# Kernel tuning notes

Hardware: AMD Instinct MI355X
Metric: run time of the kernel (lower is better)

The kernel has to match this reference:

```python
import jax, jax.numpy as jnp
import numpy as np

N_NODES = 50000
N_EDGES = 800000
F_IN = 256
F_OUT = 256


def setup_inputs() -> dict:
    key = jax.random.key(0)
    k1, k2, k3, k4, k5 = jax.random.split(key, 5)
    x = jax.random.normal(k1, (N_NODES, F_IN), dtype=jnp.float32)
    edge_index = jax.random.randint(k2, (2, N_EDGES), 0, N_NODES, dtype=jnp.int64)
    C_values = jax.random.uniform(k3, (N_EDGES,), dtype=jnp.float32)
    # nn.Linear(input_dim, output_dim) parameters
    W = jax.random.normal(k4, (F_OUT, F_IN), dtype=jnp.float32) / np.sqrt(F_IN)
    b = jax.random.normal(k5, (F_OUT,), dtype=jnp.float32) * 0.01
    return {"x": x, "edge_index": edge_index, "C_values": C_values, "W": W, "b": b}


def reference(x, edge_index, C_values, W, b):
    # gcn_norm(add_self_loops=False): deg = row-sum of edge weights,
    # w_norm[e] = deg[row]^-1/2 * w[e] * deg[col]^-1/2
    row, col = edge_index[0], edge_index[1]
    n = x.shape[0]
    deg = jax.ops.segment_sum(C_values, row, num_segments=n)  # [N]
    deg_inv_sqrt = jnp.where(deg > 0, jax.lax.rsqrt(jnp.where(deg > 0, deg, 1.0)), 0.0)
    w_norm = deg_inv_sqrt[row] * C_values * deg_inv_sqrt[col]  # [E]
    # SpMM: prop_x[i] = sum_{e: row[e]=i} w_norm[e] * x[col[e]]
    prop_x = jax.ops.segment_sum(w_norm[:, None] * x[col], row, num_segments=n)  # [N, F_in]
    # dense linear transform
    return prop_x @ W.T + b  # [N, F_out]
```

## Files before the change

### kernel.cpp

```cpp
#include <hip/hip_runtime.h>
#include <hip/hip_bf16.h>

#define NN 50000
#define NE 800000
#define FD 256
#define NN_PAD 50048
#define SCAN_B 196
#define NPB 16

typedef __attribute__((ext_vector_type(8))) short bf16x8;
typedef __attribute__((ext_vector_type(4))) float f32x4;
typedef unsigned long long ull;

__device__ __forceinline__ short f2bf(float f) {
    union { float f; unsigned u; } v; v.f = f;
    unsigned r = v.u + 0x7fffu + ((v.u >> 16) & 1u);
    return (short)(r >> 16);
}
__device__ __forceinline__ float bf2f(unsigned short u) {
    union { unsigned u; float f; } v; v.u = ((unsigned)u) << 16;
    return v.f;
}

__global__ void count_deg_kernel(const int* __restrict__ row, const float* __restrict__ cv,
                                 ull* __restrict__ dc) {
    int e = blockIdx.x * blockDim.x + threadIdx.x;
    if (e < NE) {
        int r = row[e];
        unsigned cf = (unsigned)(cv[e] * 16777216.0f + 0.5f);
        atomicAdd(&dc[r], (1ULL << 40) | (ull)cf);
    }
}

__device__ __forceinline__ int block_excl_scan256(int v, int tid) {
    __shared__ int ws[4];
    int lane = tid & 63, wv = tid >> 6;
    int incl = v;
#pragma unroll
    for (int off = 1; off < 64; off <<= 1) {
        int t = __shfl_up(incl, off);
        if (lane >= off) incl += t;
    }
    if (lane == 63) ws[wv] = incl;
    __syncthreads();
    int acc = 0;
#pragma unroll
    for (int k = 0; k < 4; ++k) if (k < wv) acc += ws[k];
    return acc + incl - v;
}

__global__ void sum_dinv_kernel(const ull* __restrict__ dc, float* __restrict__ dinv,
                                int* __restrict__ bsum) {
    int i = blockIdx.x * 256 + threadIdx.x;
    ull v = (i < NN) ? dc[i] : 0ULL;
    int cnt = (int)(v >> 40);
    ull df = v & ((1ULL << 40) - 1);
    int lane = threadIdx.x & 63, wv = threadIdx.x >> 6;
    int s = cnt;
#pragma unroll
    for (int off = 1; off < 64; off <<= 1) s += __shfl_xor(s, off);
    __shared__ int ws[4];
    if (lane == 0) ws[wv] = s;
    __syncthreads();
    if (threadIdx.x == 0) bsum[blockIdx.x] = ws[0] + ws[1] + ws[2] + ws[3];
    if (i < NN) {
        float d = (float)df * (1.0f / 16777216.0f);
        dinv[i] = (df > 0) ? rsqrtf(d) : 0.f;
    }
}

__global__ void scan_bsum_kernel(int* __restrict__ bsum) {
    int tid = threadIdx.x;
    int v = (tid < SCAN_B) ? bsum[tid] : 0;
    int excl = block_excl_scan256(v, tid);
    if (tid < SCAN_B) bsum[tid] = excl;
}

__global__ void write_rs_kernel(const ull* __restrict__ dc, const int* __restrict__ bsum,
                                int* __restrict__ rs, int* __restrict__ cursor) {
    int i = blockIdx.x * 256 + threadIdx.x;
    int v = (i < NN) ? (int)(dc[i] >> 40) : 0;
    int excl = block_excl_scan256(v, threadIdx.x) + bsum[blockIdx.x];
    if (i < NN) { rs[i] = excl; cursor[i] = excl; }
    if (i == NN - 1) rs[NN] = excl + v;
}

__global__ void quant_kernel(const float* __restrict__ x, const float* __restrict__ W,
                             const float* __restrict__ dinv, unsigned* __restrict__ q8,
                             float* __restrict__ scale, short* __restrict__ Wb) {
    int wid = blockIdx.x * 4 + (threadIdx.x >> 6);
    int lane = threadIdx.x & 63;
    if (wid < NN) {
        int r = wid;
        float dr = dinv[r];
        float4 v = *(const float4*)(x + (size_t)r * FD + lane * 4);
        v.x *= dr; v.y *= dr; v.z *= dr; v.w *= dr;
        float m = fmaxf(fmaxf(fabsf(v.x), fabsf(v.y)), fmaxf(fabsf(v.z), fabsf(v.w)));
#pragma unroll
        for (int off = 1; off < 64; off <<= 1) m = fmaxf(m, __shfl_xor(m, off, 64));
        float s   = (m > 0.f) ? m * (1.0f / 127.0f) : 1.0f;
        float inv = (m > 0.f) ? 127.0f / m : 0.f;
        if (lane == 0) scale[r] = s;
        int q0 = (int)rintf(v.x * inv) + 128;
        int q1 = (int)rintf(v.y * inv) + 128;
        int q2 = (int)rintf(v.z * inv) + 128;
        int q3 = (int)rintf(v.w * inv) + 128;
        q8[r * 64 + lane] = (unsigned)q0 | ((unsigned)q1 << 8) |
                            ((unsigned)q2 << 16) | ((unsigned)q3 << 24);
    } else {
        int j = (wid - NN) * 64 + lane;
        if (j < FD * FD) Wb[j] = f2bf(W[j]);
    }
}

__global__ void bucket_kernel(const int* __restrict__ row, const int* __restrict__ col,
                              const float* __restrict__ cv, const float* __restrict__ scale,
                              int* __restrict__ cursor, unsigned* __restrict__ e_cw) {
    int e = blockIdx.x * blockDim.x + threadIdx.x;
    if (e >= NE) return;
    int r = row[e], c = col[e];
    float w = cv[e] * scale[c];
    int idx = atomicAdd(&cursor[r], 1);
    unsigned wb = (unsigned)(unsigned short)f2bf(w);
    e_cw[idx] = (wb << 16) | (unsigned)c;
}

__global__ __launch_bounds__(256) void fused_kernel(
        const unsigned* __restrict__ q8, const unsigned* __restrict__ e_cw,
        const int* __restrict__ rs, const float* __restrict__ dinv,
        const short* __restrict__ Wb, const float* __restrict__ bias,
        float* __restrict__ out) {
    __shared__ short Ab[NPB][264];
    int tid = threadIdx.x, lane = tid & 63, wv = tid >> 6;
    int q = lane >> 4, i = lane & 15;
    int nbase = blockIdx.x * NPB;
    int n = nbase + wv * 4 + q;

    int e = rs[n], en = rs[n + 1];
    const unsigned* xq = q8 + i * 4;

    float acc[16];
#pragma unroll
    for (int k = 0; k < 16; ++k) acc[k] = 0.f;
    float wsum = 0.f;

#define EDGE(V, CW) do {                                                     \
        float w_ = bf2f((unsigned short)((CW) >> 16));                       \
        wsum += w_;                                                          \
        acc[0]  = fmaf(w_, (float)(unsigned char)((V).x      ), acc[0]);     \
        acc[1]  = fmaf(w_, (float)(unsigned char)((V).x >>  8), acc[1]);     \
        acc[2]  = fmaf(w_, (float)(unsigned char)((V).x >> 16), acc[2]);     \
        acc[3]  = fmaf(w_, (float)((V).x >> 24), acc[3]);                    \
        acc[4]  = fmaf(w_, (float)(unsigned char)((V).y      ), acc[4]);     \
        acc[5]  = fmaf(w_, (float)(unsigned char)((V).y >>  8), acc[5]);     \
        acc[6]  = fmaf(w_, (float)(unsigned char)((V).y >> 16), acc[6]);     \
        acc[7]  = fmaf(w_, (float)((V).y >> 24), acc[7]);                    \
        acc[8]  = fmaf(w_, (float)(unsigned char)((V).z      ), acc[8]);     \
        acc[9]  = fmaf(w_, (float)(unsigned char)((V).z >>  8), acc[9]);     \
        acc[10] = fmaf(w_, (float)(unsigned char)((V).z >> 16), acc[10]);    \
        acc[11] = fmaf(w_, (float)((V).z >> 24), acc[11]);                   \
        acc[12] = fmaf(w_, (float)(unsigned char)((V).w      ), acc[12]);    \
        acc[13] = fmaf(w_, (float)(unsigned char)((V).w >>  8), acc[13]);    \
        acc[14] = fmaf(w_, (float)(unsigned char)((V).w >> 16), acc[14]);    \
        acc[15] = fmaf(w_, (float)((V).w >> 24), acc[15]);                   \
    } while (0)

    while (e < en && (e & 3)) {
        unsigned cw = e_cw[e];
        uint4 v = *(const uint4*)(xq + (size_t)(cw & 0xFFFFu) * 64);
        EDGE(v, cw);
        ++e;
    }
    for (; e + 4 <= en; e += 4) {
        uint4 cw4 = *(const uint4*)(e_cw + e);
        uint4 v0 = *(const uint4*)(xq + (size_t)(cw4.x & 0xFFFFu) * 64);
        uint4 v1 = *(const uint4*)(xq + (size_t)(cw4.y & 0xFFFFu) * 64);
        uint4 v2 = *(const uint4*)(xq + (size_t)(cw4.z & 0xFFFFu) * 64);
        uint4 v3 = *(const uint4*)(xq + (size_t)(cw4.w & 0xFFFFu) * 64);
        EDGE(v0, cw4.x);
        EDGE(v1, cw4.y);
        EDGE(v2, cw4.z);
        EDGE(v3, cw4.w);
    }
    for (; e < en; ++e) {
        unsigned cw = e_cw[e];
        uint4 v = *(const uint4*)(xq + (size_t)(cw & 0xFFFFu) * 64);
        EDGE(v, cw);
    }
#undef EDGE

    {
        float dr = dinv[n];
        float base = 128.f * wsum;
        bf16x8 lo, hi;
#pragma unroll
        for (int k = 0; k < 8; ++k) {
            lo[k] = f2bf((acc[k] - base) * dr);
            hi[k] = f2bf((acc[k + 8] - base) * dr);
        }
        *(bf16x8*)&Ab[wv * 4 + q][i * 16] = lo;
        *(bf16x8*)&Ab[wv * 4 + q][i * 16 + 8] = hi;
    }
    __syncthreads();

    int m = lane & 15, g = lane >> 4;
    f32x4 acc0 = {0,0,0,0}, acc1 = {0,0,0,0}, acc2 = {0,0,0,0}, acc3 = {0,0,0,0};
    const short* w0 = Wb + (size_t)(wv * 64 + 0  + m) * FD;
    const short* w1 = Wb + (size_t)(wv * 64 + 16 + m) * FD;
    const short* w2 = Wb + (size_t)(wv * 64 + 32 + m) * FD;
    const short* w3 = Wb + (size_t)(wv * 64 + 48 + m) * FD;
#pragma unroll
    for (int ks = 0; ks < 8; ++ks) {
        int ko = ks * 32 + g * 8;
        bf16x8 af = *(const bf16x8*)&Ab[m][ko];
        bf16x8 b0 = *(const bf16x8*)(w0 + ko);
        bf16x8 b1 = *(const bf16x8*)(w1 + ko);
        bf16x8 b2 = *(const bf16x8*)(w2 + ko);
        bf16x8 b3 = *(const bf16x8*)(w3 + ko);
        acc0 = __builtin_amdgcn_mfma_f32_16x16x32_bf16(af, b0, acc0, 0, 0, 0);
        acc1 = __builtin_amdgcn_mfma_f32_16x16x32_bf16(af, b1, acc1, 0, 0, 0);
        acc2 = __builtin_amdgcn_mfma_f32_16x16x32_bf16(af, b2, acc2, 0, 0, 0);
        acc3 = __builtin_amdgcn_mfma_f32_16x16x32_bf16(af, b3, acc3, 0, 0, 0);
    }
#pragma unroll
    for (int nt = 0; nt < 4; ++nt) {
        f32x4 a = nt == 0 ? acc0 : nt == 1 ? acc1 : nt == 2 ? acc2 : acc3;
        int c = wv * 64 + nt * 16 + m;
        float bv = bias[c];
#pragma unroll
        for (int r = 0; r < 4; ++r) {
            out[(size_t)(nbase + g * 4 + r) * FD + c] = a[r] + bv;
        }
    }
}

extern "C" void kernel_launch(void* const* d_in, const int* in_sizes, int n_in,
                              void* d_out, int out_size, void* d_ws, size_t ws_size,
                              hipStream_t stream) {
    const float* x  = (const float*)d_in[0];
    const int*   ei = (const int*)d_in[1];
    const float* cv = (const float*)d_in[2];
    const float* W  = (const float*)d_in[3];
    const float* b  = (const float*)d_in[4];
    float* out = (float*)d_out;

    const int* row = ei;
    const int* col = ei + NE;

    ull*      dc     = (ull*)d_ws;
    unsigned* e_cw   = (unsigned*)(dc + NN_PAD);
    unsigned* q8     = e_cw + NE;
    short*    Wb     = (short*)(q8 + (size_t)NN * 64);
    float*    dinv   = (float*)(Wb + (size_t)FD * FD);
    float*    scale  = dinv + NN_PAD;
    int*      rs     = (int*)(scale + NN_PAD);
    int*      cursor = rs + NN_PAD;
    int*      bsum   = cursor + NN_PAD;

    hipMemsetAsync(dc, 0, NN_PAD * sizeof(ull), stream);

    count_deg_kernel<<<(NE + 255) / 256, 256, 0, stream>>>(row, cv, dc);
    sum_dinv_kernel<<<SCAN_B, 256, 0, stream>>>(dc, dinv, bsum);
    scan_bsum_kernel<<<1, 256, 0, stream>>>(bsum);
    write_rs_kernel<<<SCAN_B, 256, 0, stream>>>(dc, bsum, rs, cursor);
    quant_kernel<<<NN / 4 + 256, 256, 0, stream>>>(x, W, dinv, q8, scale, Wb);
    bucket_kernel<<<(NE + 255) / 256, 256, 0, stream>>>(row, col, cv, scale, cursor, e_cw);

    fused_kernel<<<NN / NPB, 256, 0, stream>>>(q8, e_cw, rs, dinv, Wb, b, out);
}
```

Baseline: 187.0 us.

## Fuse degree scan and quantization into single-pass look-back kernel

Replaces the three-kernel block-sum/scan/write sequence and the separate quantization kernel with one kernel that uses a decoupled look-back prefix scan, then quantizes 256 rows per block. The bf16 conversion of W is folded into the degree-count kernel. This removes several kernel launches and intermediate round trips. In exchange, quantization now runs on only 196 blocks with a serial per-wave row loop, which reduces the memory parallelism available for streaming x.

```diff
diff --git a/kernel.cpp b/kernel.cpp
--- a/kernel.cpp
+++ b/kernel.cpp
@@ -23,8 +23,10 @@
 }
 
 __global__ void count_deg_kernel(const int* __restrict__ row, const float* __restrict__ cv,
-                                 ull* __restrict__ dc) {
+                                 ull* __restrict__ dc,
+                                 const float* __restrict__ W, short* __restrict__ Wb) {
     int e = blockIdx.x * blockDim.x + threadIdx.x;
+    if (e < FD * FD) Wb[e] = f2bf(W[e]);
     if (e < NE) {
         int r = row[e];
         unsigned cf = (unsigned)(cv[e] * 16777216.0f + 0.5f);
@@ -32,7 +34,7 @@
     }
 }
 
-__device__ __forceinline__ int block_excl_scan256(int v, int tid) {
+__device__ __forceinline__ int block_scan256(int v, int tid, int* total) {
     __shared__ int ws[4];
     int lane = tid & 63, wv = tid >> 6;
     int incl = v;
@@ -46,70 +48,71 @@
     int acc = 0;
 #pragma unroll
     for (int k = 0; k < 4; ++k) if (k < wv) acc += ws[k];
+    *total = ws[0] + ws[1] + ws[2] + ws[3];
     return acc + incl - v;
 }
 
-__global__ void sum_dinv_kernel(const ull* __restrict__ dc, float* __restrict__ dinv,
-                                int* __restrict__ bsum) {
-    int i = blockIdx.x * 256 + threadIdx.x;
+__global__ void scan_quant_kernel(const ull* __restrict__ dc, const float* __restrict__ x,
+                                  ull* __restrict__ lb, float* __restrict__ dinv,
+                                  float* __restrict__ scale, int* __restrict__ rs,
+                                  int* __restrict__ cursor, unsigned* __restrict__ q8) {
+    int b = blockIdx.x, tid = threadIdx.x;
+    int i = b * 256 + tid;
+
     ull v = (i < NN) ? dc[i] : 0ULL;
     int cnt = (int)(v >> 40);
     ull df = v & ((1ULL << 40) - 1);
-    int lane = threadIdx.x & 63, wv = threadIdx.x >> 6;
-    int s = cnt;
-#pragma unroll
-    for (int off = 1; off < 64; off <<= 1) s += __shfl_xor(s, off);
-    __shared__ int ws[4];
-    if (lane == 0) ws[wv] = s;
-    __syncthreads();
-    if (threadIdx.x == 0) bsum[blockIdx.x] = ws[0] + ws[1] + ws[2] + ws[3];
     if (i < NN) {
         float d = (float)df * (1.0f / 16777216.0f);
         dinv[i] = (df > 0) ? rsqrtf(d) : 0.f;
     }
-}
-
-__global__ void scan_bsum_kernel(int* __restrict__ bsum) {
-    int tid = threadIdx.x;
-    int v = (tid < SCAN_B) ? bsum[tid] : 0;
-    int excl = block_excl_scan256(v, tid);
-    if (tid < SCAN_B) bsum[tid] = excl;
-}
-
-__global__ void write_rs_kernel(const ull* __restrict__ dc, const int* __restrict__ bsum,
-                                int* __restrict__ rs, int* __restrict__ cursor) {
-    int i = blockIdx.x * 256 + threadIdx.x;
-    int v = (i < NN) ? (int)(dc[i] >> 40) : 0;
-    int excl = block_excl_scan256(v, threadIdx.x) + bsum[blockIdx.x];
+
+    int total;
+    int excl_in = block_scan256(cnt, tid, &total);
+
+    __shared__ int sb_pref;
+    if (tid == 0) {
+        atomicExch(&lb[b], (1ULL << 62) | (unsigned)total);
+        ull run = 0;
+        for (int p = b - 1; p >= 0; --p) {
+            ull s;
+            do {
+                s = atomicAdd(&lb[p], 0ULL);
+                if ((s >> 62) == 0) __builtin_amdgcn_s_sleep(1);
+            } while ((s >> 62) == 0);
+            run += (unsigned)s;
+            if ((s >> 62) == 2) break;
+        }
+        atomicExch(&lb[b], (2ULL << 62) | (unsigned)(run + total));
+        sb_pref = (int)run;
+    }
+    __syncthreads();
+
+    int excl = sb_pref + excl_in;
     if (i < NN) { rs[i] = excl; cursor[i] = excl; }
-    if (i == NN - 1) rs[NN] = excl + v;
-}
-
-__global__ void quant_kernel(const float* __restrict__ x, const float* __restrict__ W,
-                             const float* __restrict__ dinv, unsigned* __restrict__ q8,
-                             float* __restrict__ scale, short* __restrict__ Wb) {
-    int wid = blockIdx.x * 4 + (threadIdx.x >> 6);
-    int lane = threadIdx.x & 63;
-    if (wid < NN) {
-        int r = wid;
+    if (i == NN - 1) rs[NN] = excl + cnt;
+
+    int lane = tid & 63, wv = tid >> 6;
+    int rbase = b * 256 + wv * 64;
+#pragma unroll 1
+    for (int k = 0; k < 64; ++k) {
+        int r = rbase + k;
+        if (r >= NN) break;
         float dr = dinv[r];
-        float4 v = *(const float4*)(x + (size_t)r * FD + lane * 4);
-        v.x *= dr; v.y *= dr; v.z *= dr; v.w *= dr;
-        float m = fmaxf(fmaxf(fabsf(v.x), fabsf(v.y)), fmaxf(fabsf(v.z), fabsf(v.w)));
+        float4 xv = *(const float4*)(x + (size_t)r * FD + lane * 4);
+        xv.x *= dr; xv.y *= dr; xv.z *= dr; xv.w *= dr;
+        float m = fmaxf(fmaxf(fabsf(xv.x), fabsf(xv.y)), fmaxf(fabsf(xv.z), fabsf(xv.w)));
 #pragma unroll
         for (int off = 1; off < 64; off <<= 1) m = fmaxf(m, __shfl_xor(m, off, 64));
         float s   = (m > 0.f) ? m * (1.0f / 127.0f) : 1.0f;
         float inv = (m > 0.f) ? 127.0f / m : 0.f;
         if (lane == 0) scale[r] = s;
-        int q0 = (int)rintf(v.x * inv) + 128;
-        int q1 = (int)rintf(v.y * inv) + 128;
-        int q2 = (int)rintf(v.z * inv) + 128;
-        int q3 = (int)rintf(v.w * inv) + 128;
+        int q0 = (int)rintf(xv.x * inv) + 128;
+        int q1 = (int)rintf(xv.y * inv) + 128;
+        int q2 = (int)rintf(xv.z * inv) + 128;
+        int q3 = (int)rintf(xv.w * inv) + 128;
         q8[r * 64 + lane] = (unsigned)q0 | ((unsigned)q1 << 8) |
                             ((unsigned)q2 << 16) | ((unsigned)q3 << 24);
-    } else {
-        int j = (wid - NN) * 64 + lane;
-        if (j < FD * FD) Wb[j] = f2bf(W[j]);
     }
 }
 
@@ -248,22 +251,19 @@
     const int* col = ei + NE;
 
     ull*      dc     = (ull*)d_ws;
-    unsigned* e_cw   = (unsigned*)(dc + NN_PAD);
+    ull*      lb     = dc + NN_PAD;
+    unsigned* e_cw   = (unsigned*)(lb + 256);
     unsigned* q8     = e_cw + NE;
     short*    Wb     = (short*)(q8 + (size_t)NN * 64);
     float*    dinv   = (float*)(Wb + (size_t)FD * FD);
     float*    scale  = dinv + NN_PAD;
     int*      rs     = (int*)(scale + NN_PAD);
     int*      cursor = rs + NN_PAD;
-    int*      bsum   = cursor + NN_PAD;
-
-    hipMemsetAsync(dc, 0, NN_PAD * sizeof(ull), stream);
-
-    count_deg_kernel<<<(NE + 255) / 256, 256, 0, stream>>>(row, cv, dc);
-    sum_dinv_kernel<<<SCAN_B, 256, 0, stream>>>(dc, dinv, bsum);
-    scan_bsum_kernel<<<1, 256, 0, stream>>>(bsum);
-    write_rs_kernel<<<SCAN_B, 256, 0, stream>>>(dc, bsum, rs, cursor);
-    quant_kernel<<<NN / 4 + 256, 256, 0, stream>>>(x, W, dinv, q8, scale, Wb);
+
+    hipMemsetAsync(dc, 0, (NN_PAD + 256) * sizeof(ull), stream);
+
+    count_deg_kernel<<<(NE + 255) / 256, 256, 0, stream>>>(row, cv, dc, W, Wb);
+    scan_quant_kernel<<<SCAN_B, 256, 0, stream>>>(dc, x, lb, dinv, scale, rs, cursor, q8);
     bucket_kernel<<<(NE + 255) / 256, 256, 0, stream>>>(row, col, cv, scale, cursor, e_cw);
 
     fused_kernel<<<NN / NPB, 256, 0, stream>>>(q8, e_cw, rs, dinv, Wb, b, out);
```

Result: slower. 219.9 us (+17.6%).
